# Performance work log

Measured on AMD Instinct MI355X. Metric: run time of the kernel, lower is better.

The kernel has to match this reference:

```python
import jax, jax.numpy as jnp
import numpy as np

N = 8192
STEPS = 10        # num_propagation_steps
ALPHA = 0.5       # self-retention parameter
LR = 0.01         # learning_rate for the M update
EPS = 1e-10


def setup_inputs() -> dict:
    key = jax.random.key(0)
    k1, k2 = jax.random.split(key)
    adj_matrix = jax.random.uniform(k1, (N, N), dtype=jnp.float32)  # dense non-negative adjacency
    positive_nodes = jax.random.bernoulli(k2, 0.5, (N,)).astype(jnp.float32)  # binary labels
    M = jnp.ones((N, N), dtype=jnp.float32)  # nn.Parameter initialized to ones
    return {"adj_matrix": adj_matrix, "positive_nodes": positive_nodes, "M": M}


def _propagation_loss(adj, pos):
    # degree_matrix @ adj @ degree_matrix with diagonal degree matrix ==
    # row/column scaling by deg^{-1/2} (same math, no O(N^3) diag GEMMs)
    d = jnp.power(adj.sum(axis=1), -0.5)          # [N]
    diffusion = d[:, None] * adj * d[None, :]     # [N, N]
    cp = jnp.stack([1.0 - pos, pos], axis=1)      # [N, 2] class posterior

    def step(cp, _):
        cp = ALPHA * (diffusion @ cp) + (1.0 - ALPHA) * cp
        return cp, None

    cp, _ = jax.lax.scan(step, cp, None, length=STEPS)
    # mean of -log(1 - neg_prob + eps) over nodes where positive_nodes == 1
    neg = cp[:, 0]
    loss = -(pos * jnp.log(1.0 - neg + EPS)).sum() / pos.sum()
    return loss


def reference(adj_matrix, positive_nodes, M):
    loss = _propagation_loss(adj_matrix, positive_nodes)
    # In the original, loss.backward() populates M.grad; since the loss does not
    # depend on M, dLoss/dM == 0, so M_new = M - LR * 0 = M (math-equivalent).
    updated_adj = M * adj_matrix
    return updated_adj, loss
```

## Files before the change

### kernel.cpp

```cpp
#include <hip/hip_runtime.h>
#include <hip/hip_bf16.h>

#define NN 8192
constexpr int   STEPS = 10;
constexpr float ALPHA = 0.5f;
constexpr float EPSV  = 1e-10f;

typedef float f32x2 __attribute__((ext_vector_type(2)));
typedef float f32x4 __attribute__((ext_vector_type(4)));

static __device__ __forceinline__ unsigned int f2bf(float f) {
    unsigned int u = __float_as_uint(f);
    return (u + 0x7FFFu + ((u >> 16) & 1u)) >> 16;
}
static __device__ __forceinline__ float bf2f(unsigned int h) {
    return __uint_as_float(h << 16);
}

__global__ __launch_bounds__(256) void k_fused_prep(
        const float* __restrict__ adj, const float* __restrict__ M,
        float* __restrict__ out, unsigned char* __restrict__ a8,
        float* __restrict__ rowsum) {
    const int row = blockIdx.x;
    const int t   = threadIdx.x;
    const float* arow = adj + (size_t)row * NN;
    const float* mrow = M   + (size_t)row * NN;
    float*       orow = out + (size_t)row * NN;
    unsigned char* brow = a8 + (size_t)row * NN;
    float acc = 0.0f;
#pragma unroll
    for (int g = 0; g < 2; ++g) {
        f32x4 v[4], m[4];
#pragma unroll
        for (int k = 0; k < 4; ++k) {
            const int j = (g * 4 + k) * 1024 + t * 4;
            v[k] = __builtin_nontemporal_load((const f32x4*)(arow + j));
        }
#pragma unroll
        for (int k = 0; k < 4; ++k) {
            const int j = (g * 4 + k) * 1024 + t * 4;
            m[k] = __builtin_nontemporal_load((const f32x4*)(mrow + j));
        }
#pragma unroll
        for (int k = 0; k < 4; ++k) {
            const int j = (g * 4 + k) * 1024 + t * 4;
            f32x4 r = v[k] * m[k];
            __builtin_nontemporal_store(r, (f32x4*)(orow + j));
            acc += (v[k].x + v[k].y) + (v[k].z + v[k].w);
            int p = __builtin_amdgcn_cvt_pk_fp8_f32(v[k].x, v[k].y, 0, false);
            p     = __builtin_amdgcn_cvt_pk_fp8_f32(v[k].z, v[k].w, p, true);
            *(unsigned int*)(brow + j) = (unsigned int)p;
        }
    }
#pragma unroll
    for (int o = 32; o > 0; o >>= 1) acc += __shfl_down(acc, o);
    __shared__ float red[4];
    if ((t & 63) == 0) red[t >> 6] = acc;
    __syncthreads();
    if (t == 0) rowsum[row] = (red[0] + red[1]) + (red[2] + red[3]);
}

#define CBLK  256
#define CROWS 32
#define RREG  16
#define RLDS  16

static __device__ __forceinline__ void gbar(unsigned int* flags, unsigned int phase) {
    __syncthreads();
    if (threadIdx.x == 0)
        __hip_atomic_store(&flags[blockIdx.x], phase, __ATOMIC_RELEASE,
                           __HIP_MEMORY_SCOPE_AGENT);
    while (__hip_atomic_load(&flags[threadIdx.x], __ATOMIC_ACQUIRE,
                             __HIP_MEMORY_SCOPE_AGENT) < phase)
        __builtin_amdgcn_s_sleep(1);
    __syncthreads();
}

static __device__ __forceinline__ int lds_off(int r, int c) {
    return r * 8192 + ((c ^ ((c >> 3) & 7)) << 4);
}

#define FMA_WORD(w, m)                                                \
    { f32x2 lo = __builtin_amdgcn_cvt_pk_f32_fp8((int)(w), false);    \
      f32x2 hi = __builtin_amdgcn_cvt_pk_f32_fp8((int)(w), true);     \
      a01 += lo * zf2[(m)];                                           \
      a23 += hi * zf2[(m) + 1]; }

#define DOT_ROW(q0, q1, res)                                                        \
    { f32x2 a01 = {0.f, 0.f}, a23 = {0.f, 0.f};                                     \
      FMA_WORD(q0.x, 0)  FMA_WORD(q0.y, 2)  FMA_WORD(q0.z, 4)  FMA_WORD(q0.w, 6)   \
      FMA_WORD(q1.x, 8)  FMA_WORD(q1.y, 10) FMA_WORD(q1.z, 12) FMA_WORD(q1.w, 14)  \
      res = (a01[0] + a01[1]) + (a23[0] + a23[1]); }

__global__ __launch_bounds__(256, 1) void k_chain(
        const unsigned char* __restrict__ a8, const float* __restrict__ rowsum,
        const float* __restrict__ pos,
        unsigned int* __restrict__ z_a, unsigned int* __restrict__ z_b,
        unsigned int* __restrict__ flags, float* __restrict__ accs,
        float* __restrict__ loss_out) {
    const int t  = threadIdx.x;
    const int b  = blockIdx.x;
    const int r0 = b * CROWS;

    __shared__ __align__(16) unsigned char lds_a[RLDS * 8192];
    __shared__ float xloc[CROWS], dloc[CROWS], ploc[CROWS];
    __shared__ unsigned short zs[CROWS];
    __shared__ float red[CROWS][4];

    if (t < CROWS) {
        const int row = r0 + t;
        const float dv = rsqrtf(rowsum[row]);
        const float pv = pos[row];
        const float xv = 1.0f - pv;
        dloc[t] = dv; ploc[t] = pv; xloc[t] = xv;
        zs[t] = (unsigned short)f2bf(dv * xv);
    }
    __syncthreads();
    if (t < CROWS / 2) {
        unsigned int w = (unsigned)zs[2 * t] | ((unsigned)zs[2 * t + 1] << 16);
        __hip_atomic_store(&z_a[r0 / 2 + t], w, __ATOMIC_RELAXED,
                           __HIP_MEMORY_SCOPE_AGENT);
    }

    const int j = t * 32;
    uint4 pa[RREG][2];
#pragma unroll
    for (int r = 0; r < RREG; ++r) {
        const unsigned char* arow = a8 + (size_t)(r0 + r) * NN + j;
        pa[r][0] = *(const uint4*)(arow);
        pa[r][1] = *(const uint4*)(arow + 16);
    }
#pragma unroll
    for (int g = 0; g < 4; ++g) {
        uint4 v0[4], v1[4];
#pragma unroll
        for (int rr = 0; rr < 4; ++rr) {
            const unsigned char* arow =
                a8 + (size_t)(r0 + RREG + g * 4 + rr) * NN + j;
            v0[rr] = *(const uint4*)(arow);
            v1[rr] = *(const uint4*)(arow + 16);
        }
#pragma unroll
        for (int rr = 0; rr < 4; ++rr) {
            const int lr = g * 4 + rr;
            *(uint4*)&lds_a[lds_off(lr, 2 * t)]     = v0[rr];
            *(uint4*)&lds_a[lds_off(lr, 2 * t + 1)] = v1[rr];
        }
    }
    gbar(flags, 1u);

    const unsigned int* zi = z_a;
    unsigned int*       zo = z_b;
#pragma unroll 1
    for (int s = 0; s < STEPS; ++s) {
        f32x2 zf2[16];
        {
            const uint4* zv = (const uint4*)(zi + t * 16);
            uint4 zq[4];
#pragma unroll
            for (int k = 0; k < 4; ++k) zq[k] = zv[k];
#pragma unroll
            for (int k = 0; k < 4; ++k) {
                const unsigned int ww[4] = {zq[k].x, zq[k].y, zq[k].z, zq[k].w};
#pragma unroll
                for (int m = 0; m < 4; ++m) {
                    f32x2 p;
                    p[0] = bf2f(ww[m] & 0xFFFFu);
                    p[1] = bf2f(ww[m] >> 16);
                    zf2[k * 4 + m] = p;
                }
            }
        }
        float accA[RREG];
#pragma unroll
        for (int r = 0; r < RREG; ++r) {
            DOT_ROW(pa[r][0], pa[r][1], accA[r]);
        }
#pragma unroll
        for (int r = 0; r < RREG; ++r) {
#pragma unroll
            for (int o = 32; o > 0; o >>= 1) accA[r] += __shfl_down(accA[r], o);
        }
        if ((t & 63) == 0) {
            const int w = t >> 6;
#pragma unroll
            for (int r = 0; r < RREG; ++r) red[r][w] = accA[r];
        }
        float accB[RLDS];
#pragma unroll
        for (int r = 0; r < RLDS; ++r) {
            const uint4 q0 = *(const uint4*)&lds_a[lds_off(r, 2 * t)];
            const uint4 q1 = *(const uint4*)&lds_a[lds_off(r, 2 * t + 1)];
            DOT_ROW(q0, q1, accB[r]);
            if ((r & 3) == 3) __builtin_amdgcn_sched_barrier(0);
        }
#pragma unroll
        for (int r = 0; r < RLDS; ++r) {
#pragma unroll
            for (int o = 32; o > 0; o >>= 1) accB[r] += __shfl_down(accB[r], o);
        }
        if ((t & 63) == 0) {
            const int w = t >> 6;
#pragma unroll
            for (int r = 0; r < RLDS; ++r) red[RREG + r][w] = accB[r];
        }
        __syncthreads();
        if (t < CROWS) {
            const float y  = (red[t][0] + red[t][1]) + (red[t][2] + red[t][3]);
            const float dv = dloc[t];
            const float xn = ALPHA * dv * y + (1.0f - ALPHA) * xloc[t];
            xloc[t] = xn;
            zs[t] = (unsigned short)f2bf(dv * xn);
        }
        __syncthreads();
        if (s < STEPS - 1) {
            if (t < CROWS / 2) {
                unsigned int w = (unsigned)zs[2 * t] | ((unsigned)zs[2 * t + 1] << 16);
                __hip_atomic_store(&zo[r0 / 2 + t], w, __ATOMIC_RELAXED,
                                   __HIP_MEMORY_SCOPE_AGENT);
            }
            gbar(flags, (unsigned)(2 + s));
            const unsigned int* tz = zi; zi = zo; zo = (unsigned int*)tz;
        }
    }

    if (t < CROWS) {
        const float xn = xloc[t];
        red[t][0] = ploc[t] * logf(1.0f - xn + EPSV);
        red[t][1] = ploc[t];
    }
    __syncthreads();
    if (t == 0) {
        float n = 0.0f, dd = 0.0f;
#pragma unroll
        for (int r = 0; r < CROWS; ++r) { n += red[r][0]; dd += red[r][1]; }
        atomicAdd(&accs[0], n);
        atomicAdd(&accs[1], dd);
        unsigned int tk = __hip_atomic_fetch_add((unsigned int*)&accs[2], 1u,
                                                 __ATOMIC_ACQ_REL,
                                                 __HIP_MEMORY_SCOPE_AGENT);
        if (tk == CBLK - 1) {
            float sn = __hip_atomic_load(&accs[0], __ATOMIC_RELAXED,
                                         __HIP_MEMORY_SCOPE_AGENT);
            float sd = __hip_atomic_load(&accs[1], __ATOMIC_RELAXED,
                                         __HIP_MEMORY_SCOPE_AGENT);
            loss_out[0] = -sn / sd;
        }
    }
}

__global__ __launch_bounds__(256) void k_rowsum(
        const float* __restrict__ adj, float* __restrict__ rowsum) {
    const int row = blockIdx.x;
    const int t   = threadIdx.x;
    const float* arow = adj + (size_t)row * NN;
    float acc = 0.0f;
#pragma unroll
    for (int c = 0; c < 8; ++c) {
        const int j = c * 1024 + t * 4;
        float4 v = *(const float4*)(arow + j);
        acc += (v.x + v.y) + (v.z + v.w);
    }
#pragma unroll
    for (int o = 32; o > 0; o >>= 1) acc += __shfl_down(acc, o);
    __shared__ float red[4];
    if ((t & 63) == 0) red[t >> 6] = acc;
    __syncthreads();
    if (t == 0) rowsum[row] = (red[0] + red[1]) + (red[2] + red[3]);
}

__global__ __launch_bounds__(256) void k_init(
        const float* __restrict__ rowsum, const float* __restrict__ pos,
        float* __restrict__ d, float* __restrict__ x,
        unsigned short* __restrict__ zbf, float* __restrict__ zf) {
    const int i = blockIdx.x * 256 + threadIdx.x;
    const float dv = rsqrtf(rowsum[i]);
    const float xv = 1.0f - pos[i];
    const float zv = dv * xv;
    d[i] = dv;
    x[i] = xv;
    zbf[i] = (unsigned short)f2bf(zv);
    zf[i] = zv;
}

__global__ __launch_bounds__(256) void k_step_fp8(
        const unsigned char* __restrict__ a8, const float* __restrict__ d,
        const float* __restrict__ xin, const unsigned short* __restrict__ zin,
        float* __restrict__ xout, unsigned short* __restrict__ zout) {
    const int r0 = blockIdx.x * 4;
    const int t  = threadIdx.x;
    const int j  = t * 32;

    uint4 pa[4][2];
#pragma unroll
    for (int r = 0; r < 4; ++r) {
        const unsigned char* arow = a8 + (size_t)(r0 + r) * NN + j;
        pa[r][0] = *(const uint4*)(arow);
        pa[r][1] = *(const uint4*)(arow + 16);
    }
    uint4 zp[4];
#pragma unroll
    for (int k = 0; k < 4; ++k)
        zp[k] = *(const uint4*)(zin + j + 8 * k);

    float acc0 = 0.0f, acc1 = 0.0f, acc2 = 0.0f, acc3 = 0.0f;
#pragma unroll
    for (int h = 0; h < 2; ++h) {
        float zf[16];
#pragma unroll
        for (int k = 0; k < 2; ++k) {
            uint4 q = zp[2 * h + k];
            zf[k * 8 + 0] = bf2f(q.x & 0xFFFFu); zf[k * 8 + 1] = bf2f(q.x >> 16);
            zf[k * 8 + 2] = bf2f(q.y & 0xFFFFu); zf[k * 8 + 3] = bf2f(q.y >> 16);
            zf[k * 8 + 4] = bf2f(q.z & 0xFFFFu); zf[k * 8 + 5] = bf2f(q.z >> 16);
            zf[k * 8 + 6] = bf2f(q.w & 0xFFFFu); zf[k * 8 + 7] = bf2f(q.w >> 16);
        }
#pragma unroll
        for (int r = 0; r < 4; ++r) {
            const uint4 p = pa[r][h];
            unsigned int w[4] = {p.x, p.y, p.z, p.w};
            float a = 0.0f;
#pragma unroll
            for (int wi = 0; wi < 4; ++wi) {
                f32x2 lo = __builtin_amdgcn_cvt_pk_f32_fp8((int)w[wi], false);
                f32x2 hi = __builtin_amdgcn_cvt_pk_f32_fp8((int)w[wi], true);
                a = fmaf(lo[0], zf[wi * 4 + 0], a);
                a = fmaf(lo[1], zf[wi * 4 + 1], a);
                a = fmaf(hi[0], zf[wi * 4 + 2], a);
                a = fmaf(hi[1], zf[wi * 4 + 3], a);
            }
            if (r == 0) acc0 += a; else if (r == 1) acc1 += a;
            else if (r == 2) acc2 += a; else acc3 += a;
        }
    }
#pragma unroll
    for (int o = 32; o > 0; o >>= 1) {
        acc0 += __shfl_down(acc0, o);
        acc1 += __shfl_down(acc1, o);
        acc2 += __shfl_down(acc2, o);
        acc3 += __shfl_down(acc3, o);
    }
    __shared__ float red[4][4];
    if ((t & 63) == 0) {
        const int w = t >> 6;
        red[0][w] = acc0; red[1][w] = acc1; red[2][w] = acc2; red[3][w] = acc3;
    }
    __syncthreads();
    if (t < 4) {
        const int row = r0 + t;
        const float y  = (red[t][0] + red[t][1]) + (red[t][2] + red[t][3]);
        const float dv = d[row];
        const float xn = ALPHA * dv * y + (1.0f - ALPHA) * xin[row];
        xout[row] = xn;
        zout[row] = (unsigned short)f2bf(dv * xn);
    }
}

__global__ __launch_bounds__(256) void k_step_f32(
        const float* __restrict__ adj, const float* __restrict__ d,
        const float* __restrict__ xin, const float* __restrict__ zin,
        float* __restrict__ xout, float* __restrict__ zout) {
    const int row = blockIdx.x;
    const int t   = threadIdx.x;
    const float* arow = adj + (size_t)row * NN;
    float acc = 0.0f;
#pragma unroll
    for (int c = 0; c < 8; ++c) {
        const int j = c * 1024 + t * 4;
        float4 a = *(const float4*)(arow + j);
        float4 z = *(const float4*)(zin + j);
        acc = fmaf(a.x, z.x, acc); acc = fmaf(a.y, z.y, acc);
        acc = fmaf(a.z, z.z, acc); acc = fmaf(a.w, z.w, acc);
    }
#pragma unroll
    for (int o = 32; o > 0; o >>= 1) acc += __shfl_down(acc, o);
    __shared__ float red[4];
    if ((t & 63) == 0) red[t >> 6] = acc;
    __syncthreads();
    if (t == 0) {
        const float y  = (red[0] + red[1]) + (red[2] + red[3]);
        const float dv = d[row];
        const float xn = ALPHA * dv * y + (1.0f - ALPHA) * xin[row];
        xout[row] = xn;
        zout[row] = dv * xn;
    }
}

__global__ __launch_bounds__(256) void k_mul(
        const float* __restrict__ adj, const float* __restrict__ M,
        float* __restrict__ out) {
    size_t i = ((size_t)blockIdx.x * blockDim.x + threadIdx.x) * 4;
    const size_t stride = (size_t)gridDim.x * blockDim.x * 4;
    const size_t total = (size_t)NN * NN;
    for (; i < total; i += stride) {
        float4 a = *(const float4*)(adj + i);
        float4 m = *(const float4*)(M + i);
        float4 r;
        r.x = a.x * m.x; r.y = a.y * m.y; r.z = a.z * m.z; r.w = a.w * m.w;
        *(float4*)(out + i) = r;
    }
}

__global__ __launch_bounds__(1024) void k_loss(
        const float* __restrict__ pos, const float* __restrict__ xfin,
        float* __restrict__ out) {
    const int t = threadIdx.x;
    float sn = 0.0f, sd = 0.0f;
#pragma unroll
    for (int c = 0; c < 8; ++c) {
        const int i4 = c * 1024 + t;
        float4 p = *(const float4*)(pos  + i4 * 4);
        float4 x = *(const float4*)(xfin + i4 * 4);
        sn += p.x * logf(1.0f - x.x + EPSV);
        sn += p.y * logf(1.0f - x.y + EPSV);
        sn += p.z * logf(1.0f - x.z + EPSV);
        sn += p.w * logf(1.0f - x.w + EPSV);
        sd += (p.x + p.y) + (p.z + p.w);
    }
#pragma unroll
    for (int o = 32; o > 0; o >>= 1) {
        sn += __shfl_down(sn, o);
        sd += __shfl_down(sd, o);
    }
    __shared__ float rn[16], rd[16];
    if ((t & 63) == 0) { rn[t >> 6] = sn; rd[t >> 6] = sd; }
    __syncthreads();
    if (t == 0) {
        float n = 0.0f, dd = 0.0f;
#pragma unroll
        for (int k = 0; k < 16; ++k) { n += rn[k]; dd += rd[k]; }
        out[0] = -n / dd;
    }
}

extern "C" void kernel_launch(void* const* d_in, const int* in_sizes, int n_in,
                              void* d_out, int out_size, void* d_ws, size_t ws_size,
                              hipStream_t stream) {
    const float* adj = (const float*)d_in[0];
    const float* pos = (const float*)d_in[1];
    const float* M   = (const float*)d_in[2];
    float* out = (float*)d_out;

    char* ws = (char*)d_ws;
    float* d_vec  = (float*)(ws + 0);
    float* rowsum = (float*)(ws + 32768);
    float* x_a    = (float*)(ws + 65536);
    float* x_b    = (float*)(ws + 98304);
    unsigned short* zb_a = (unsigned short*)(ws + 131072);
    unsigned short* zb_b = (unsigned short*)(ws + 163840);
    unsigned int* flags  = (unsigned int*)(ws + 196608);
    float*        accs   = (float*)(ws + 196608 + 4096);
    float* zf_a   = (float*)(ws + 196608);
    float* zf_b   = (float*)(ws + 229376);
    unsigned char* a8 = (unsigned char*)(ws + 262144);

    const size_t need_fp8 = 262144 + (size_t)NN * NN;
    const bool use_fp8 = (ws_size >= need_fp8);

    static int s_chain = -1;
    if (s_chain < 0) {
        int nb = 0, ncu = 0;
        hipError_t e1 = hipOccupancyMaxActiveBlocksPerMultiprocessor(&nb, k_chain, 256, 0);
        hipError_t e2 = hipDeviceGetAttribute(&ncu, hipDeviceAttributeMultiprocessorCount, 0);
        s_chain = (e1 == hipSuccess && e2 == hipSuccess && nb >= 1 && nb * ncu >= CBLK) ? 1 : 0;
    }

    if (use_fp8) {
        k_fused_prep<<<NN, 256, 0, stream>>>(adj, M, out, a8, rowsum);
    } else {
        k_rowsum<<<NN, 256, 0, stream>>>(adj, rowsum);
    }

    if (use_fp8 && s_chain == 1) {
        hipMemsetAsync(flags, 0, 4096 + 64, stream);
        k_chain<<<CBLK, 256, 0, stream>>>(a8, rowsum, pos,
                                          (unsigned int*)zb_a, (unsigned int*)zb_b,
                                          flags, accs, out + (size_t)NN * NN);
        return;
    }

    k_init<<<NN / 256, 256, 0, stream>>>(rowsum, pos, d_vec, x_a, zb_a, zf_a);
    float* xi = x_a; float* xo = x_b;
    unsigned short* zbi = zb_a; unsigned short* zbo = zb_b;
    float* zfi = zf_a; float* zfo = zf_b;
    for (int s = 0; s < STEPS; ++s) {
        if (use_fp8) {
            k_step_fp8<<<NN / 4, 256, 0, stream>>>(a8, d_vec, xi, zbi, xo, zbo);
            unsigned short* tz = zbi; zbi = zbo; zbo = tz;
        } else {
            k_step_f32<<<NN, 256, 0, stream>>>(adj, d_vec, xi, zfi, xo, zfo);
            float* tz = zfi; zfi = zfo; zfo = tz;
        }
        float* t = xi; xi = xo; xo = t;
    }
    if (!use_fp8) {
        k_mul<<<2048, 256, 0, stream>>>(adj, M, out);
    }
    k_loss<<<1, 1024, 0, stream>>>(pos, xi, out + (size_t)NN * NN);
}
```

Measured before the change: 261.0 us.

## Replace flag-array grid barrier with single atomic counter and drop occupancy fallback

The grid barrier moves from per-block flag stores, polled by every thread, to one atomic counter. Only thread 0 increments it and polls with a longer sleep and a timeout escape. The z vector reads become relaxed atomic loads instead of vector loads, and the host occupancy check and the fp8 multi-kernel fallback are removed, so the persistent chain kernel always runs when the workspace fits. A tiny kernel zeroes the counter instead of a memset. The aim is to cut barrier contention and launch overhead, at the cost of possible deadlock or timeout if not all 256 blocks are co-resident, and of scalar z loads.

```diff
diff --git a/kernel.cpp b/kernel.cpp
--- a/kernel.cpp
+++ b/kernel.cpp
@@ -60,19 +60,26 @@
     if (t == 0) rowsum[row] = (red[0] + red[1]) + (red[2] + red[3]);
 }
 
+__global__ __launch_bounds__(64) void k_zero(unsigned int* __restrict__ p) {
+    if (threadIdx.x < 16) p[threadIdx.x] = 0u;
+}
+
 #define CBLK  256
 #define CROWS 32
 #define RREG  16
 #define RLDS  16
 
-static __device__ __forceinline__ void gbar(unsigned int* flags, unsigned int phase) {
-    __syncthreads();
-    if (threadIdx.x == 0)
-        __hip_atomic_store(&flags[blockIdx.x], phase, __ATOMIC_RELEASE,
-                           __HIP_MEMORY_SCOPE_AGENT);
-    while (__hip_atomic_load(&flags[threadIdx.x], __ATOMIC_ACQUIRE,
-                             __HIP_MEMORY_SCOPE_AGENT) < phase)
-        __builtin_amdgcn_s_sleep(1);
+static __device__ __forceinline__ void gbar(unsigned int* ctr, unsigned int target) {
+    __syncthreads();
+    if (threadIdx.x == 0) {
+        __hip_atomic_fetch_add(ctr, 1u, __ATOMIC_ACQ_REL, __HIP_MEMORY_SCOPE_AGENT);
+        const long long t0 = clock64();
+        while (__hip_atomic_load(ctr, __ATOMIC_ACQUIRE,
+                                 __HIP_MEMORY_SCOPE_AGENT) < target) {
+            __builtin_amdgcn_s_sleep(16);
+            if (clock64() - t0 > 400000000LL) break;
+        }
+    }
     __syncthreads();
 }
 
@@ -96,7 +103,7 @@
         const unsigned char* __restrict__ a8, const float* __restrict__ rowsum,
         const float* __restrict__ pos,
         unsigned int* __restrict__ z_a, unsigned int* __restrict__ z_b,
-        unsigned int* __restrict__ flags, float* __restrict__ accs,
+        unsigned int* __restrict__ ctr, float* __restrict__ accs,
         float* __restrict__ loss_out) {
     const int t  = threadIdx.x;
     const int b  = blockIdx.x;
@@ -147,7 +154,7 @@
             *(uint4*)&lds_a[lds_off(lr, 2 * t + 1)] = v1[rr];
         }
     }
-    gbar(flags, 1u);
+    gbar(ctr, 1u * CBLK);
 
     const unsigned int* zi = z_a;
     unsigned int*       zo = z_b;
@@ -155,20 +162,15 @@
     for (int s = 0; s < STEPS; ++s) {
         f32x2 zf2[16];
         {
-            const uint4* zv = (const uint4*)(zi + t * 16);
-            uint4 zq[4];
-#pragma unroll
-            for (int k = 0; k < 4; ++k) zq[k] = zv[k];
-#pragma unroll
-            for (int k = 0; k < 4; ++k) {
-                const unsigned int ww[4] = {zq[k].x, zq[k].y, zq[k].z, zq[k].w};
-#pragma unroll
-                for (int m = 0; m < 4; ++m) {
-                    f32x2 p;
-                    p[0] = bf2f(ww[m] & 0xFFFFu);
-                    p[1] = bf2f(ww[m] >> 16);
-                    zf2[k * 4 + m] = p;
-                }
+            const int zbase = t * 16;
+#pragma unroll
+            for (int k = 0; k < 16; ++k) {
+                const unsigned int q = __hip_atomic_load(
+                    &zi[zbase + k], __ATOMIC_RELAXED, __HIP_MEMORY_SCOPE_AGENT);
+                f32x2 p;
+                p[0] = bf2f(q & 0xFFFFu);
+                p[1] = bf2f(q >> 16);
+                zf2[k] = p;
             }
         }
         float accA[RREG];
@@ -219,7 +221,7 @@
                 __hip_atomic_store(&zo[r0 / 2 + t], w, __ATOMIC_RELAXED,
                                    __HIP_MEMORY_SCOPE_AGENT);
             }
-            gbar(flags, (unsigned)(2 + s));
+            gbar(ctr, (unsigned)(2 + s) * CBLK);
             const unsigned int* tz = zi; zi = zo; zo = (unsigned int*)tz;
         }
     }
@@ -271,89 +273,13 @@
 
 __global__ __launch_bounds__(256) void k_init(
         const float* __restrict__ rowsum, const float* __restrict__ pos,
-        float* __restrict__ d, float* __restrict__ x,
-        unsigned short* __restrict__ zbf, float* __restrict__ zf) {
+        float* __restrict__ d, float* __restrict__ x, float* __restrict__ zf) {
     const int i = blockIdx.x * 256 + threadIdx.x;
     const float dv = rsqrtf(rowsum[i]);
     const float xv = 1.0f - pos[i];
-    const float zv = dv * xv;
     d[i] = dv;
     x[i] = xv;
-    zbf[i] = (unsigned short)f2bf(zv);
-    zf[i] = zv;
-}
-
-__global__ __launch_bounds__(256) void k_step_fp8(
-        const unsigned char* __restrict__ a8, const float* __restrict__ d,
-        const float* __restrict__ xin, const unsigned short* __restrict__ zin,
-        float* __restrict__ xout, unsigned short* __restrict__ zout) {
-    const int r0 = blockIdx.x * 4;
-    const int t  = threadIdx.x;
-    const int j  = t * 32;
-
-    uint4 pa[4][2];
-#pragma unroll
-    for (int r = 0; r < 4; ++r) {
-        const unsigned char* arow = a8 + (size_t)(r0 + r) * NN + j;
-        pa[r][0] = *(const uint4*)(arow);
-        pa[r][1] = *(const uint4*)(arow + 16);
-    }
-    uint4 zp[4];
-#pragma unroll
-    for (int k = 0; k < 4; ++k)
-        zp[k] = *(const uint4*)(zin + j + 8 * k);
-
-    float acc0 = 0.0f, acc1 = 0.0f, acc2 = 0.0f, acc3 = 0.0f;
-#pragma unroll
-    for (int h = 0; h < 2; ++h) {
-        float zf[16];
-#pragma unroll
-        for (int k = 0; k < 2; ++k) {
-            uint4 q = zp[2 * h + k];
-            zf[k * 8 + 0] = bf2f(q.x & 0xFFFFu); zf[k * 8 + 1] = bf2f(q.x >> 16);
-            zf[k * 8 + 2] = bf2f(q.y & 0xFFFFu); zf[k * 8 + 3] = bf2f(q.y >> 16);
-            zf[k * 8 + 4] = bf2f(q.z & 0xFFFFu); zf[k * 8 + 5] = bf2f(q.z >> 16);
-            zf[k * 8 + 6] = bf2f(q.w & 0xFFFFu); zf[k * 8 + 7] = bf2f(q.w >> 16);
-        }
-#pragma unroll
-        for (int r = 0; r < 4; ++r) {
-            const uint4 p = pa[r][h];
-            unsigned int w[4] = {p.x, p.y, p.z, p.w};
-            float a = 0.0f;
-#pragma unroll
-            for (int wi = 0; wi < 4; ++wi) {
-                f32x2 lo = __builtin_amdgcn_cvt_pk_f32_fp8((int)w[wi], false);
-                f32x2 hi = __builtin_amdgcn_cvt_pk_f32_fp8((int)w[wi], true);
-                a = fmaf(lo[0], zf[wi * 4 + 0], a);
-                a = fmaf(lo[1], zf[wi * 4 + 1], a);
-                a = fmaf(hi[0], zf[wi * 4 + 2], a);
-                a = fmaf(hi[1], zf[wi * 4 + 3], a);
-            }
-            if (r == 0) acc0 += a; else if (r == 1) acc1 += a;
-            else if (r == 2) acc2 += a; else acc3 += a;
-        }
-    }
-#pragma unroll
-    for (int o = 32; o > 0; o >>= 1) {
-        acc0 += __shfl_down(acc0, o);
-        acc1 += __shfl_down(acc1, o);
-        acc2 += __shfl_down(acc2, o);
-        acc3 += __shfl_down(acc3, o);
-    }
-    __shared__ float red[4][4];
-    if ((t & 63) == 0) {
-        const int w = t >> 6;
-        red[0][w] = acc0; red[1][w] = acc1; red[2][w] = acc2; red[3][w] = acc3;
-    }
-    __syncthreads();
-    if (t < 4) {
-        const int row = r0 + t;
-        const float y  = (red[t][0] + red[t][1]) + (red[t][2] + red[t][3]);
-        const float dv = d[row];
-        const float xn = ALPHA * dv * y + (1.0f - ALPHA) * xin[row];
-        xout[row] = xn;
-        zout[row] = (unsigned short)f2bf(dv * xn);
-    }
+    zf[i] = dv * xv;
 }
 
 __global__ __launch_bounds__(256) void k_step_f32(
@@ -446,55 +372,34 @@
     float* rowsum = (float*)(ws + 32768);
     float* x_a    = (float*)(ws + 65536);
     float* x_b    = (float*)(ws + 98304);
-    unsigned short* zb_a = (unsigned short*)(ws + 131072);
-    unsigned short* zb_b = (unsigned short*)(ws + 163840);
-    unsigned int* flags  = (unsigned int*)(ws + 196608);
-    float*        accs   = (float*)(ws + 196608 + 4096);
-    float* zf_a   = (float*)(ws + 196608);
+    unsigned int* z_a    = (unsigned int*)(ws + 131072);
+    unsigned int* z_b    = (unsigned int*)(ws + 163840);
+    unsigned int* ctr    = (unsigned int*)(ws + 196608);
+    float*        accs   = (float*)(ws + 196608 + 16);
+    float* zf_a   = (float*)(ws + 212992);
     float* zf_b   = (float*)(ws + 229376);
     unsigned char* a8 = (unsigned char*)(ws + 262144);
 
     const size_t need_fp8 = 262144 + (size_t)NN * NN;
     const bool use_fp8 = (ws_size >= need_fp8);
 
-    static int s_chain = -1;
-    if (s_chain < 0) {
-        int nb = 0, ncu = 0;
-        hipError_t e1 = hipOccupancyMaxActiveBlocksPerMultiprocessor(&nb, k_chain, 256, 0);
-        hipError_t e2 = hipDeviceGetAttribute(&ncu, hipDeviceAttributeMultiprocessorCount, 0);
-        s_chain = (e1 == hipSuccess && e2 == hipSuccess && nb >= 1 && nb * ncu >= CBLK) ? 1 : 0;
-    }
-
     if (use_fp8) {
+        k_zero<<<1, 64, 0, stream>>>(ctr);
         k_fused_prep<<<NN, 256, 0, stream>>>(adj, M, out, a8, rowsum);
-    } else {
-        k_rowsum<<<NN, 256, 0, stream>>>(adj, rowsum);
-    }
-
-    if (use_fp8 && s_chain == 1) {
-        hipMemsetAsync(flags, 0, 4096 + 64, stream);
-        k_chain<<<CBLK, 256, 0, stream>>>(a8, rowsum, pos,
-                                          (unsigned int*)zb_a, (unsigned int*)zb_b,
-                                          flags, accs, out + (size_t)NN * NN);
+        k_chain<<<CBLK, 256, 0, stream>>>(a8, rowsum, pos, z_a, z_b,
+                                          ctr, accs, out + (size_t)NN * NN);
         return;
     }
 
-    k_init<<<NN / 256, 256, 0, stream>>>(rowsum, pos, d_vec, x_a, zb_a, zf_a);
+    k_rowsum<<<NN, 256, 0, stream>>>(adj, rowsum);
+    k_init<<<NN / 256, 256, 0, stream>>>(rowsum, pos, d_vec, x_a, zf_a);
     float* xi = x_a; float* xo = x_b;
-    unsigned short* zbi = zb_a; unsigned short* zbo = zb_b;
     float* zfi = zf_a; float* zfo = zf_b;
     for (int s = 0; s < STEPS; ++s) {
-        if (use_fp8) {
-            k_step_fp8<<<NN / 4, 256, 0, stream>>>(a8, d_vec, xi, zbi, xo, zbo);
-            unsigned short* tz = zbi; zbi = zbo; zbo = tz;
-        } else {
-            k_step_f32<<<NN, 256, 0, stream>>>(adj, d_vec, xi, zfi, xo, zfo);
-            float* tz = zfi; zfi = zfo; zfo = tz;
-        }
+        k_step_f32<<<NN, 256, 0, stream>>>(adj, d_vec, xi, zfi, xo, zfo);
+        float* tz = zfi; zfi = zfo; zfo = tz;
         float* t = xi; xi = xo; xo = t;
     }
-    if (!use_fp8) {
-        k_mul<<<2048, 256, 0, stream>>>(adj, M, out);
-    }
+    k_mul<<<2048, 256, 0, stream>>>(adj, M, out);
     k_loss<<<1, 1024, 0, stream>>>(pos, xi, out + (size_t)NN * NN);
 }
```

Measured after the change: 442.1 us. +69.4%, slower.
